# Performance work log

Measured on AMD Instinct MI355X. Metric: run time of the kernel, lower is better.

The kernel has to match this reference:

```python
import jax, jax.numpy as jnp
import numpy as np

MAP_W = 500
INTERP_H, INTERP_W = 1024, 2048


def _bilinear_ac(x, out_h, out_w):
    # torch F.interpolate(mode='bilinear', align_corners=True), separable
    N, C, H, W = x.shape
    ys = jnp.linspace(0.0, H - 1, out_h)
    y0 = jnp.floor(ys).astype(jnp.int32)
    y1 = jnp.minimum(y0 + 1, H - 1)
    wy = (ys - y0.astype(x.dtype))[None, None, :, None]
    rows = x[:, :, y0, :] * (1 - wy) + x[:, :, y1, :] * wy  # (N,C,out_h,W)
    xs = jnp.linspace(0.0, W - 1, out_w)
    x0 = jnp.floor(xs).astype(jnp.int32)
    x1 = jnp.minimum(x0 + 1, W - 1)
    wx = (xs - x0.astype(x.dtype))[None, None, None, :]
    return rows[:, :, :, x0] * (1 - wx) + rows[:, :, :, x1] * wx


def _conv(x, w, pad):
    return jax.lax.conv_general_dilated(x, w, (1, 1), [(pad, pad), (pad, pad)],
                                        dimension_numbers=('NCHW', 'OIHW', 'NCHW'))


def _bn_relu(x, g, b):
    # BatchNorm2d in training mode: biased batch stats over (N,H,W)
    mu = jnp.mean(x, axis=(0, 2, 3), keepdims=True)
    var = jnp.var(x, axis=(0, 2, 3), keepdims=True)
    xn = (x - mu) * jax.lax.rsqrt(var + 1e-5)
    return jax.nn.relu(xn * g[None, :, None, None] + b[None, :, None, None])


def setup_inputs() -> dict:
    key = jax.random.key(0)
    ks = jax.random.split(key, 24)
    C, NOBJ = 64, 21
    features = jax.random.normal(ks[0], (1, 1, C, 256, 512), dtype=jnp.float32)
    proj_indices = jax.random.randint(ks[1], (1, MAP_W * MAP_W), 0, 400000, dtype=jnp.int64)
    masks_inliers = jax.random.bernoulli(ks[2], 0.5, (1, INTERP_H, INTERP_W))
    rgb_no_norm = jax.random.uniform(ks[3], (1, INTERP_H, INTERP_W, 3), dtype=jnp.float32) * 255.0
    def cw(k, o, i, kh, kw):
        return jax.random.normal(k, (o, i, kh, kw), dtype=jnp.float32) * (1.0 / np.sqrt(i * kh * kw))
    return {
        'features': features, 'proj_indices': proj_indices,
        'masks_inliers': masks_inliers, 'rgb_no_norm': rgb_no_norm,
        'w1': cw(ks[4], 128, C, 7, 7), 'g1': jnp.ones(128), 'b1': jnp.zeros(128),
        'w2': cw(ks[5], 64, 128, 3, 3), 'g2': jnp.ones(64), 'b2': jnp.zeros(64),
        'w3': cw(ks[6], 48, 64, 3, 3), 'g3': jnp.ones(48), 'b3': jnp.zeros(48),
        'w4': cw(ks[7], 48, 48, 3, 3), 'g4': jnp.ones(48), 'b4': jnp.zeros(48),
        'w5': cw(ks[8], NOBJ, 48, 1, 1), 'b5': jnp.zeros(NOBJ),
    }


def reference(features, proj_indices, masks_inliers, rgb_no_norm,
              w1, g1, b1, w2, g2, b2, w3, g3, b3, w4, g4, b4, w5, b5):
    N, T, C, H, W = features.shape  # N = 1
    feat = _bilinear_ac(features[:, 0], INTERP_H, INTERP_W)      # (N,C,1024,2048)
    feat = feat.transpose(0, 2, 3, 1).reshape(-1, C)             # row-major NHWC flatten
    rgb_flat = rgb_no_norm.reshape(-1, 3)
    mask_flat = masks_inliers.reshape(-1)
    # stable compaction: inlier pixels first, in original row-major order
    # (equivalent to torch boolean-mask gather feature[mask_inliers, :])
    order = jnp.argsort((~mask_flat).astype(jnp.int32), stable=True)
    compact_f = feat[order]
    compact_rgb = rgb_flat[order]
    idx = proj_indices.reshape(-1)
    m = idx < jnp.max(idx)                                       # sentinel = max value
    state = jnp.where(m[:, None], compact_f[idx], 0.0)           # replace-mode scatter
    state_rgb = jnp.where(m[:, None], compact_rgb[idx], 0.0)
    rgb_write = state_rgb.reshape(MAP_W, MAP_W, 3)
    observed_masks = m.reshape(N, MAP_W, MAP_W)
    memory = state.reshape(N, MAP_W, MAP_W, C).transpose(0, 3, 1, 2)
    # decoder (first conv in_channels fixed to C to match memory)
    x = _bn_relu(_conv(memory, w1, 3), g1, b1)
    x = _bn_relu(_conv(x, w2, 1), g2, b2)
    x = _bn_relu(_conv(x, w3, 1), g3, b3)
    x = _bn_relu(_conv(x, w4, 1), g4, b4)
    semmap = _conv(x, w5, 0) + b5[None, :, None, None]
    return (semmap, observed_masks, rgb_write)
```

## Files before the change

kernel.cpp:

```cpp
#include <hip/hip_runtime.h>

#define MAPN 250000
#define NPIX 2097152

typedef unsigned short ushort_t;
typedef __attribute__((ext_vector_type(8))) short short8;
typedef __attribute__((ext_vector_type(4))) float f32x4;

__device__ inline ushort_t f2bf(float f){
  unsigned u = __float_as_uint(f);
  u = (u + 0x7fffu + ((u >> 16) & 1u)) >> 16;
  return (ushort_t)u;
}
__device__ inline float bf2f(ushort_t h){ return __uint_as_float(((unsigned)h) << 16); }

__device__ __forceinline__ void glds16(const void* g, void* l){
  __builtin_amdgcn_global_load_lds((const __attribute__((address_space(1))) unsigned int*)g,
                                   (__attribute__((address_space(3))) unsigned int*)l, 16, 0, 0);
}

__device__ inline int read_mask(const void* p, int i, int t){
  if (t==0) return ((const int*)p)[i] != 0;
  if (t==1) return ((const unsigned char*)p)[i] != 0;
  if (t==3) return ((const long long*)p)[i] != 0;
  return ((const float*)p)[i] != 0.0f;
}
__device__ inline int read_idx(const void* p, int i, int t){
  if (t==1) return (int)((const long long*)p)[i];
  return ((const int*)p)[i];
}

__global__ void detect_kernel(const int* __restrict__ mask_w, const int* __restrict__ idx_w,
                              int* __restrict__ flags){
  int tid = threadIdx.x;
  int orv=0, modd=0, inz=0;
  for (int i=tid;i<4096;i+=256) orv |= mask_w[i];
  for (int i=tid;i<2048;i+=256) modd += (mask_w[2*i+1]!=0);
  for (int i=tid;i<2048;i+=256) inz  += (idx_w[2*i+1]!=0);
  __shared__ int sOr[256], sM[256], sI[256];
  sOr[tid]=orv; sM[tid]=modd; sI[tid]=inz; __syncthreads();
  for (int o=128;o;o>>=1){ if(tid<o){ sOr[tid]|=sOr[tid+o]; sM[tid]+=sM[tid+o]; sI[tid]+=sI[tid+o]; } __syncthreads(); }
  if (tid==0){
    int o = sOr[0];
    int mt;
    if ((o & ~1) == 0)               mt = (sM[0] > 0) ? 0 : 3;
    else if ((o & ~0x01010101) == 0) mt = 1;
    else                             mt = 2;
    flags[0] = mt;
    flags[1] = (sI[0] > 0) ? 0 : 1;
  }
}

__global__ void feat_transpose(const float* __restrict__ f, ushort_t* __restrict__ out){
  __shared__ float tile[64][65];
  int tid = threadIdx.x;
  int y = blockIdx.y;
  int x0 = blockIdx.x * 64;
  #pragma unroll
  for (int pass=0; pass<16; pass++){
    int c = pass*4 + (tid>>6);
    int x = x0 + (tid & 63);
    tile[c][tid & 63] = f[(size_t)c*131072 + (size_t)y*512 + x];
  }
  __syncthreads();
  #pragma unroll
  for (int pass=0; pass<16; pass++){
    int xl = pass*4 + (tid>>6);
    int c  = tid & 63;
    out[((size_t)y*512 + x0 + xl)*64 + c] = f2bf(tile[c][xl]);
  }
}

__global__ void scan_count(const void* __restrict__ mask, const int* __restrict__ flags,
                           int* __restrict__ blkSums){
  int t = flags[0];
  int tid = threadIdx.x;
  int base = blockIdx.x*1024 + tid*4;
  int s = 0;
  #pragma unroll
  for (int j=0;j<4;j++) s += read_mask(mask, base+j, t);
  __shared__ int red[256];
  red[tid] = s; __syncthreads();
  for (int o=128;o;o>>=1){ if (tid<o) red[tid]+=red[tid+o]; __syncthreads(); }
  if (tid==0) blkSums[blockIdx.x] = red[0];
}

__global__ void scan_offsets(const int* __restrict__ blkSums, int* __restrict__ blkOffs){
  __shared__ int tsum[256];
  int tid = threadIdx.x;
  int loc[8]; int s=0;
  #pragma unroll
  for (int j=0;j<8;j++){ loc[j]=blkSums[tid*8+j]; s+=loc[j]; }
  tsum[tid]=s; __syncthreads();
  for (int o=1;o<256;o<<=1){
    int v = (tid>=o)? tsum[tid-o] : 0;
    __syncthreads();
    tsum[tid] += v;
    __syncthreads();
  }
  int run = tsum[tid]-s;
  #pragma unroll
  for (int j=0;j<8;j++){ blkOffs[tid*8+j]=run; run+=loc[j]; }
  if (tid==255) blkOffs[2048]=run;
}

__global__ void build_table(const void* __restrict__ mask, const int* __restrict__ flags,
                            const int* __restrict__ blkOffs, int* __restrict__ table){
  int t = flags[0];
  int tid = threadIdx.x;
  int base = blockIdx.x*1024 + tid*4;
  int mv[4]; int s=0;
  #pragma unroll
  for (int j=0;j<4;j++){ mv[j]=read_mask(mask, base+j, t); s+=mv[j]; }
  __shared__ int red[256];
  red[tid]=s; __syncthreads();
  for (int o=1;o<256;o<<=1){
    int v = (tid>=o)? red[tid-o] : 0;
    __syncthreads();
    red[tid]+=v;
    __syncthreads();
  }
  int excl = red[tid]-s + blkOffs[blockIdx.x];
  int total = blkOffs[2048];
  #pragma unroll
  for (int j=0;j<4;j++){
    int p = base+j;
    int pos;
    if (mv[j]){ pos = excl; excl++; }
    else      { pos = total + (p - excl); }
    table[pos] = p;
  }
}

__global__ void max_idx_kernel(const void* __restrict__ idxp, const int* __restrict__ flags,
                               int* __restrict__ mx){
  int t = flags[1];
  int m = 0;
  for (int i = blockIdx.x*blockDim.x + threadIdx.x; i < MAPN; i += gridDim.x*blockDim.x)
    m = max(m, read_idx(idxp, i, t));
  #pragma unroll
  for (int o=32;o;o>>=1) m = max(m, __shfl_down(m, o));
  if ((threadIdx.x & 63) == 0) atomicMax(mx, m);
}

__global__ void gather_kernel(const void* __restrict__ idxp, const int* __restrict__ flags,
                              const int* __restrict__ mxp, const int* __restrict__ table,
                              const ushort_t* __restrict__ Fhwc, const float* __restrict__ rgb,
                              ushort_t* __restrict__ memory, float* __restrict__ out_obs,
                              float* __restrict__ out_rgb){
  int cell = blockIdx.x*4 + (threadIdx.x>>6);
  int lane = threadIdx.x & 63;
  int t = flags[1];
  int mx = *mxp;
  int idx = read_idx(idxp, cell, t);
  bool m = idx < mx;
  float v = 0.0f, r = 0.0f;
  if (m){
    int p = table[idx];
    int py = p >> 11, px = p & 2047;
    float fy = py * (255.0f/1023.0f);
    int y0 = (int)fy; float wy = fy - (float)y0; int y1 = min(y0+1, 255);
    float fx = px * (511.0f/2047.0f);
    int x0 = (int)fx; float wx = fx - (float)x0; int x1 = min(x0+1, 511);
    const ushort_t* f00 = Fhwc + ((size_t)y0*512 + x0)*64;
    const ushort_t* f01 = Fhwc + ((size_t)y0*512 + x1)*64;
    const ushort_t* f10 = Fhwc + ((size_t)y1*512 + x0)*64;
    const ushort_t* f11 = Fhwc + ((size_t)y1*512 + x1)*64;
    float w00=(1.0f-wy)*(1.0f-wx), w01=(1.0f-wy)*wx, w10=wy*(1.0f-wx), w11=wy*wx;
    v = w00*bf2f(f00[lane]) + w01*bf2f(f01[lane]) + w10*bf2f(f10[lane]) + w11*bf2f(f11[lane]);
    if (lane < 3) r = rgb[(size_t)p*3 + lane];
  }
  memory[(size_t)cell*64 + lane] = f2bf(v);
  if (lane == 0) out_obs[cell] = m ? 1.0f : 0.0f;
  if (lane < 3)  out_rgb[(size_t)cell*3 + lane] = r;
}

__global__ void wprep_frag2(const float* __restrict__ w, ushort_t* __restrict__ out,
                            int O, int I, int KK, int COS, int KC){
  int NFS = COS/16;
  int total = KK*KC*NFS*512;
  for (int e = blockIdx.x*blockDim.x + threadIdx.x; e < total; e += gridDim.x*blockDim.x){
    int j = e & 7, l = (e>>3)&63;
    int f = e >> 9;
    int nf = f % NFS; f /= NFS;
    int kc = f % KC;  int t = f / KC;
    int co = nf*16 + (l&15);
    int ci = kc*32 + ((l>>4)&3)*8 + j;
    float v = (co < O && ci < I) ? w[((size_t)co*I + ci)*KK + t] : 0.0f;
    out[e] = f2bf(v);
  }
}

template<int CI, int CO, int COPAD, int KS, int PAD, bool HASBN, int CIREAL,
         int TR, int WM, int WN>
__global__ __launch_bounds__(256, 2) void conv2d(const ushort_t* __restrict__ in,
                                                 const ushort_t* __restrict__ wt,
                                                 const float* __restrict__ scsh,
                                                 ushort_t* __restrict__ out,
                                                 float* __restrict__ partials){
  constexpr int TCOL = 64;
  constexpr int ECOL = TCOL + 2*PAD;
  constexpr int E    = TR*ECOL;
  constexpr int MF   = TR*4;
  constexpr int MI   = MF/WM;
  constexpr int NFS  = CO/16;
  constexpr int NFW  = NFS/WN;
  constexpr int KC   = CI/32;
  constexpr int CIG  = CI/8;
  constexpr int TB   = CO*CI*2;
  constexpr int NSL  = TB/1024;
  constexpr int NT   = KS*KS;
  constexpr int TOT  = E*CIG;
  constexpr int PASSES = (TOT+255)/256;
  constexpr int SCN = HASBN ? CIREAL : 1;

  __shared__ char sA[E*CI*2];
  __shared__ char sB[2][TB];
  __shared__ float sStat[4][NFW][16][2];
  __shared__ float sSc[SCN], sSh[SCN];

  const int tid = threadIdx.x, lane = tid & 63, wv = tid >> 6;
  const int wm = wv / WN, wn = wv % WN;
  const int cc = blockIdx.x & 7;
  const int rb = blockIdx.x >> 3;
  const int x0 = cc*TCOL, yb = rb*TR;

  if (HASBN){
    for (int i=tid;i<CIREAL;i+=256){ sSc[i]=scsh[i]; sSh[i]=scsh[CIREAL+i]; }
    __syncthreads();
  }

  int ebase[MI], frow[MI], fcolb[MI];
  #pragma unroll
  for (int mi=0;mi<MI;mi++){
    int f = wm*MI + mi;
    frow[mi]  = f >> 2;
    fcolb[mi] = (f & 3) * 16;
    ebase[mi] = frow[mi]*ECOL + fcolb[mi] + (lane & 15);
  }

  f32x4 acc[MI][NFW];
  #pragma unroll
  for (int mi=0;mi<MI;mi++)
    #pragma unroll
    for (int ni=0;ni<NFW;ni++) acc[mi][ni] = (f32x4)0.0f;

  for (int s=wv; s<NSL; s+=4)
    glds16((const char*)wt + (size_t)s*1024 + lane*16, &sB[0][s*1024]);

  int cur = 0;

  for (int kh=0; kh<KS; kh++){
    #pragma unroll
    for (int i=0;i<PASSES;i++){
      int c = i*256 + tid;
      if ((TOT % 256 == 0) || c < TOT){
        int e = c / CIG, ci8 = (c % CIG)*8;
        int row = e / ECOL, col = e % ECOL;
        int yy = yb + row + kh - PAD;
        int xx = x0 + col - PAD;
        uint4 v = make_uint4(0u,0u,0u,0u);
        bool ok = ((unsigned)yy < 500u) && ((unsigned)xx < 500u) && (!HASBN || ci8 < CIREAL);
        if (ok){
          v = *(const uint4*)(in + ((size_t)yy*500 + xx)*CI + ci8);
          if (HASBN){
            ushort_t* hv = (ushort_t*)&v;
            #pragma unroll
            for (int j=0;j<8;j++){
              float f = bf2f(hv[j]);
              f = fmaxf(fmaf(f, sSc[ci8+j], sSh[ci8+j]), 0.0f);
              hv[j] = f2bf(f);
            }
          }
        }
        unsigned wa = ((unsigned)((e*CI + ci8)*2)) ^ ((unsigned)(e&7)<<4);
        *(uint4*)(sA + wa) = v;
      }
    }
    __syncthreads();

    for (int kw=0; kw<KS; kw++){
      int t = kh*KS + kw;
      if (t+1 < NT){
        for (int s=wv; s<NSL; s+=4)
          glds16((const char*)wt + (size_t)(t+1)*TB + (size_t)s*1024 + lane*16,
                 &sB[cur^1][s*1024]);
      }
      #pragma unroll
      for (int kc=0;kc<KC;kc++){
        short8 bfr[NFW];
        #pragma unroll
        for (int ni=0;ni<NFW;ni++)
          bfr[ni] = *(const short8*)(&sB[cur][((kc*NFS + wn*NFW + ni)<<10) + lane*16]);
        #pragma unroll
        for (int mi=0;mi<MI;mi++){
          int e = ebase[mi] + kw;
          unsigned ra = ((unsigned)((e*CI + kc*32 + (lane>>4)*8)*2)) ^ ((unsigned)(e&7)<<4);
          short8 af = *(const short8*)(sA + ra);
          #pragma unroll
          for (int ni=0;ni<NFW;ni++)
            acc[mi][ni] = __builtin_amdgcn_mfma_f32_16x16x32_bf16(af, bfr[ni], acc[mi][ni], 0,0,0);
        }
      }
      __syncthreads();
      cur ^= 1;
    }
  }

  #pragma unroll
  for (int ni=0;ni<NFW;ni++){
    float ps=0.f, pq=0.f;
    #pragma unroll
    for (int mi=0;mi<MI;mi++){
      int colb = fcolb[mi] + (lane>>4)*4;
      size_t rowoff = (size_t)(yb + frow[mi])*500;
      #pragma unroll
      for (int j=0;j<4;j++){
        float v = acc[mi][ni][j];
        int colAbs = x0 + colb + j;
        if (colAbs < 500){
          ps += v; pq += v*v;
          out[(rowoff + colAbs)*COPAD + wn*(NFW*16) + ni*16 + (lane&15)] = f2bf(v);
        }
      }
    }
    ps += __shfl_xor(ps, 16); pq += __shfl_xor(pq, 16);
    ps += __shfl_xor(ps, 32); pq += __shfl_xor(pq, 32);
    if (lane < 16){ sStat[wv][ni][lane][0]=ps; sStat[wv][ni][lane][1]=pq; }
  }
  __syncthreads();
  if (tid < CO){
    int wn_ = tid / (NFW*16);
    int r = tid % (NFW*16);
    int ni_ = r >> 4, col = r & 15;
    float s = 0.f, q = 0.f;
    #pragma unroll
    for (int m=0;m<WM;m++){
      s += sStat[m*WN + wn_][ni_][col][0];
      q += sStat[m*WN + wn_][ni_][col][1];
    }
    partials[(size_t)blockIdx.x*(2*CO) + tid]      = s;
    partials[(size_t)blockIdx.x*(2*CO) + CO + tid] = q;
  }
}

__global__ void bn_reduce2(const float* __restrict__ partials, int nblk, int CO,
                           const float* __restrict__ g, const float* __restrict__ b,
                           float* __restrict__ scsh){
  int c = blockIdx.x;
  float s=0.f, q=0.f;
  for (int i=threadIdx.x; i<nblk; i+=256){
    s += partials[(size_t)i*(2*CO) + c];
    q += partials[(size_t)i*(2*CO) + CO + c];
  }
  __shared__ float rs[256], rq[256];
  rs[threadIdx.x]=s; rq[threadIdx.x]=q; __syncthreads();
  for (int o=128;o;o>>=1){
    if (threadIdx.x<o){ rs[threadIdx.x]+=rs[threadIdx.x+o]; rq[threadIdx.x]+=rq[threadIdx.x+o]; }
    __syncthreads();
  }
  if (threadIdx.x==0){
    float mean = rs[0]*(1.0f/(float)MAPN);
    float var  = rq[0]*(1.0f/(float)MAPN) - mean*mean;
    float inv  = rsqrtf(var + 1e-5f);
    float sc   = g[c]*inv;
    scsh[c]    = sc;
    scsh[CO+c] = b[c] - mean*sc;
  }
}

__global__ void conv5_kernel(const ushort_t* __restrict__ in, const float* __restrict__ w,
                             const float* __restrict__ bias, const float* __restrict__ scsh,
                             float* __restrict__ out){
  __shared__ float sw[21*48];
  __shared__ float sb[21];
  __shared__ float sc[48], sh[48];
  for (int i=threadIdx.x;i<1008;i+=256) sw[i]=w[i];
  if (threadIdx.x<21) sb[threadIdx.x]=bias[threadIdx.x];
  if (threadIdx.x<48){ sc[threadIdx.x]=scsh[threadIdx.x]; sh[threadIdx.x]=scsh[48+threadIdx.x]; }
  __syncthreads();
  int pix = blockIdx.x*256 + threadIdx.x;
  if (pix >= MAPN) return;
  float acc[21];
  #pragma unroll
  for (int i=0;i<21;i++) acc[i]=0.0f;
  const ushort_t* ip = in + (size_t)pix*64;
  #pragma unroll
  for (int cg=0; cg<6; cg++){
    uint4 v = *(const uint4*)(ip + cg*8);
    ushort_t* hv = (ushort_t*)&v;
    #pragma unroll
    for (int j=0;j<8;j++){
      int ci = cg*8+j;
      float s = fmaxf(fmaf(bf2f(hv[j]), sc[ci], sh[ci]), 0.0f);
      #pragma unroll
      for (int co=0;co<21;co++) acc[co]=fmaf(s, sw[co*48+ci], acc[co]);
    }
  }
  #pragma unroll
  for (int co=0;co<21;co++) out[(size_t)co*MAPN + pix] = acc[co] + sb[co];
}

static inline size_t al256(size_t x){ return (x + 255) & ~(size_t)255; }

extern "C" void kernel_launch(void* const* d_in, const int* in_sizes, int n_in,
                              void* d_out, int out_size, void* d_ws, size_t ws_size,
                              hipStream_t stream){
  const float* features = (const float*)d_in[0];
  const void*  proj     = d_in[1];
  const void*  mask     = d_in[2];
  const float* rgb      = (const float*)d_in[3];
  const float* w1 = (const float*)d_in[4];
  const float* g1 = (const float*)d_in[5];
  const float* b1 = (const float*)d_in[6];
  const float* w2 = (const float*)d_in[7];
  const float* g2 = (const float*)d_in[8];
  const float* b2 = (const float*)d_in[9];
  const float* w3 = (const float*)d_in[10];
  const float* g3 = (const float*)d_in[11];
  const float* b3 = (const float*)d_in[12];
  const float* w4 = (const float*)d_in[13];
  const float* g4 = (const float*)d_in[14];
  const float* b4 = (const float*)d_in[15];
  const float* w5 = (const float*)d_in[16];
  const float* b5 = (const float*)d_in[17];

  char* ws = (char*)d_ws;
  size_t off = 0;
  ushort_t* mem_bf = (ushort_t*)(ws + off); off += al256((size_t)MAPN*64*2);
  ushort_t* actA   = (ushort_t*)(ws + off); off += al256((size_t)MAPN*128*2);
  ushort_t* actB   = (ushort_t*)(ws + off); off += al256((size_t)MAPN*64*2);
  ushort_t* Fhwc   = (ushort_t*)(ws + off); off += al256((size_t)131072*64*2);
  int*      table  = (int*)(ws + off);      off += al256((size_t)NPIX*4);
  ushort_t* wh1    = (ushort_t*)(ws + off); off += al256((size_t)128*49*64*2);
  ushort_t* wh2    = (ushort_t*)(ws + off); off += al256((size_t)64*9*128*2);
  ushort_t* wh3    = (ushort_t*)(ws + off); off += al256((size_t)48*9*64*2);
  ushort_t* wh4    = (ushort_t*)(ws + off); off += al256((size_t)48*9*64*2);
  float*    partials = (float*)(ws + off);  off += al256((size_t)2048*256*4);
  int* blkSums = (int*)(ws + off); off += al256(2048*4);
  int* blkOffs = (int*)(ws + off); off += al256(2049*4);
  int* maxidx  = (int*)(ws + off); off += 256;
  int* flags   = (int*)(ws + off); off += 256;
  float* scsh1 = (float*)(ws + off); off += al256(256*4);
  float* scsh2 = (float*)(ws + off); off += al256(256*4);
  float* scsh3 = (float*)(ws + off); off += al256(256*4);
  float* scsh4 = (float*)(ws + off); off += al256(256*4);

  float* out_sem = (float*)d_out;
  float* out_obs = out_sem + (size_t)21*MAPN;
  float* out_rgb = out_obs + MAPN;

  detect_kernel<<<1,256,0,stream>>>((const int*)mask, (const int*)proj, flags);
  feat_transpose<<<dim3(8,256),256,0,stream>>>(features, Fhwc);

  scan_count<<<2048,256,0,stream>>>(mask, flags, blkSums);
  scan_offsets<<<1,256,0,stream>>>(blkSums, blkOffs);
  build_table<<<2048,256,0,stream>>>(mask, flags, blkOffs, table);

  hipMemsetAsync(maxidx, 0, 4, stream);
  max_idx_kernel<<<256,256,0,stream>>>(proj, flags, maxidx);

  wprep_frag2<<<512,256,0,stream>>>(w1, wh1, 128, 64, 49, 128, 2);
  wprep_frag2<<<128,256,0,stream>>>(w2, wh2, 64, 128, 9, 64, 4);
  wprep_frag2<<<64,256,0,stream>>>(w3, wh3, 48, 64, 9, 48, 2);
  wprep_frag2<<<64,256,0,stream>>>(w4, wh4, 48, 48, 9, 48, 2);

  gather_kernel<<<62500,256,0,stream>>>(proj, flags, maxidx, table, Fhwc, rgb,
                                        mem_bf, out_obs, out_rgb);

  conv2d<64,128,128,7,3,false,64,4,2,2><<<125*8,256,0,stream>>>(mem_bf, wh1, nullptr, actA, partials);
  bn_reduce2<<<128,256,0,stream>>>(partials, 1000, 128, g1, b1, scsh1);

  conv2d<128,64,64,3,1,true,128,2,2,2><<<250*8,256,0,stream>>>(actA, wh2, scsh1, actB, partials);
  bn_reduce2<<<64,256,0,stream>>>(partials, 2000, 64, g2, b2, scsh2);

  conv2d<64,48,64,3,1,true,64,4,4,1><<<125*8,256,0,stream>>>(actB, wh3, scsh2, actA, partials);
  bn_reduce2<<<48,256,0,stream>>>(partials, 1000, 48, g3, b3, scsh3);

  conv2d<64,48,64,3,1,true,48,4,4,1><<<125*8,256,0,stream>>>(actA, wh4, scsh3, actB, partials);
  bn_reduce2<<<48,256,0,stream>>>(partials, 1000, 48, g4, b4, scsh4);

  conv5_kernel<<<(MAPN+255)/256,256,0,stream>>>(actB, w5, b5, scsh4, out_sem);
}
```

Baseline: 479.3 us.

## Run decoder convolutions with FP8 MFMA using per-channel scaled weights

Converts the gathered memory map, the BN-applied activations and the conv weights to FP8 (e4m3) and switches the conv MFMAs from bf16 16x16x32 to fp8 16x16x32. Weights get a per-output-channel power-of-two scale, which the following training-mode BatchNorm cancels. The aim is to halve LDS and global traffic for activations and weights and to use the higher FP8 matrix throughput. It also doubles the conv2 row tile and folds the max-index memset into the detect kernel. The cost is a large precision drop that may break output tolerance.

```diff
diff --git a/kernel.cpp b/kernel.cpp
--- a/kernel.cpp
+++ b/kernel.cpp
@@ -4,7 +4,6 @@
 #define NPIX 2097152
 
 typedef unsigned short ushort_t;
-typedef __attribute__((ext_vector_type(8))) short short8;
 typedef __attribute__((ext_vector_type(4))) float f32x4;
 
 __device__ inline ushort_t f2bf(float f){
@@ -31,7 +30,7 @@
 }
 
 __global__ void detect_kernel(const int* __restrict__ mask_w, const int* __restrict__ idx_w,
-                              int* __restrict__ flags){
+                              int* __restrict__ flags, int* __restrict__ maxidx){
   int tid = threadIdx.x;
   int orv=0, modd=0, inz=0;
   for (int i=tid;i<4096;i+=256) orv |= mask_w[i];
@@ -48,6 +47,7 @@
     else                             mt = 2;
     flags[0] = mt;
     flags[1] = (sI[0] > 0) ? 0 : 1;
+    maxidx[0] = 0;
   }
 }
 
@@ -146,7 +146,7 @@
 __global__ void gather_kernel(const void* __restrict__ idxp, const int* __restrict__ flags,
                               const int* __restrict__ mxp, const int* __restrict__ table,
                               const ushort_t* __restrict__ Fhwc, const float* __restrict__ rgb,
-                              ushort_t* __restrict__ memory, float* __restrict__ out_obs,
+                              unsigned char* __restrict__ mem_f8, float* __restrict__ out_obs,
                               float* __restrict__ out_rgb){
   int cell = blockIdx.x*4 + (threadIdx.x>>6);
   int lane = threadIdx.x & 63;
@@ -170,34 +170,49 @@
     v = w00*bf2f(f00[lane]) + w01*bf2f(f01[lane]) + w10*bf2f(f10[lane]) + w11*bf2f(f11[lane]);
     if (lane < 3) r = rgb[(size_t)p*3 + lane];
   }
-  memory[(size_t)cell*64 + lane] = f2bf(v);
+  int q = __builtin_amdgcn_cvt_pk_fp8_f32(v, 0.0f, 0, false);
+  mem_f8[(size_t)cell*64 + lane] = (unsigned char)(q & 0xff);
   if (lane == 0) out_obs[cell] = m ? 1.0f : 0.0f;
   if (lane < 3)  out_rgb[(size_t)cell*3 + lane] = r;
 }
 
-__global__ void wprep_frag2(const float* __restrict__ w, ushort_t* __restrict__ out,
-                            int O, int I, int KK, int COS, int KC){
-  int NFS = COS/16;
-  int total = KK*KC*NFS*512;
-  for (int e = blockIdx.x*blockDim.x + threadIdx.x; e < total; e += gridDim.x*blockDim.x){
-    int j = e & 7, l = (e>>3)&63;
-    int f = e >> 9;
-    int nf = f % NFS; f /= NFS;
-    int kc = f % KC;  int t = f / KC;
-    int co = nf*16 + (l&15);
-    int ci = kc*32 + ((l>>4)&3)*8 + j;
-    float v = (co < O && ci < I) ? w[((size_t)co*I + ci)*KK + t] : 0.0f;
-    out[e] = f2bf(v);
+__global__ void wprep_f8(const float* __restrict__ w, unsigned char* __restrict__ out,
+                         int O, int I, int CIPAD, int KK){
+  int co = blockIdx.x;
+  int n = KK*CIPAD;
+  int NFS = (O+15)>>4;
+  int KC  = CIPAD>>5;
+  float mx = 0.f;
+  for (int e=threadIdx.x; e<n; e+=256){
+    int ci = e % CIPAD;
+    if (ci < I){
+      int t = e / CIPAD;
+      mx = fmaxf(mx, fabsf(w[((size_t)co*I + ci)*KK + t]));
+    }
+  }
+  __shared__ float red[256];
+  red[threadIdx.x]=mx; __syncthreads();
+  for (int o=128;o;o>>=1){ if(threadIdx.x<o) red[threadIdx.x]=fmaxf(red[threadIdx.x],red[threadIdx.x+o]); __syncthreads(); }
+  float m = red[0];
+  float sc = (m > 0.f) ? exp2f(floorf(log2f(224.0f/m))) : 1.0f;
+  for (int e=threadIdx.x; e<n; e+=256){
+    int t = e / CIPAD, ci = e % CIPAD;
+    float v = (ci < I) ? w[((size_t)co*I + ci)*KK + t]*sc : 0.0f;
+    int q = __builtin_amdgcn_cvt_pk_fp8_f32(v, 0.0f, 0, false);
+    int kc = ci>>5, g=(ci>>3)&3, j=ci&7;
+    int l = g*16 + (co&15);
+    size_t pos = ((size_t)(t*KC + kc)*NFS + (co>>4))*512 + l*8 + j;
+    out[pos] = (unsigned char)(q & 0xff);
   }
 }
 
 template<int CI, int CO, int COPAD, int KS, int PAD, bool HASBN, int CIREAL,
          int TR, int WM, int WN>
-__global__ __launch_bounds__(256, 2) void conv2d(const ushort_t* __restrict__ in,
-                                                 const ushort_t* __restrict__ wt,
-                                                 const float* __restrict__ scsh,
-                                                 ushort_t* __restrict__ out,
-                                                 float* __restrict__ partials){
+__global__ __launch_bounds__(256, 2) void conv2d_f8(const void* __restrict__ in,
+                                                    const unsigned char* __restrict__ wt,
+                                                    const float* __restrict__ scsh,
+                                                    ushort_t* __restrict__ out,
+                                                    float* __restrict__ partials){
   constexpr int TCOL = 64;
   constexpr int ECOL = TCOL + 2*PAD;
   constexpr int E    = TR*ECOL;
@@ -207,15 +222,15 @@
   constexpr int NFW  = NFS/WN;
   constexpr int KC   = CI/32;
   constexpr int CIG  = CI/8;
-  constexpr int TB   = CO*CI*2;
+  constexpr int TB   = CO*CI;
   constexpr int NSL  = TB/1024;
   constexpr int NT   = KS*KS;
   constexpr int TOT  = E*CIG;
   constexpr int PASSES = (TOT+255)/256;
   constexpr int SCN = HASBN ? CIREAL : 1;
 
-  __shared__ char sA[E*CI*2];
-  __shared__ char sB[2][TB];
+  __shared__ unsigned char sA[E*CI];
+  __shared__ unsigned char sB[2][TB];
   __shared__ float sStat[4][NFW][16][2];
   __shared__ float sSc[SCN], sSh[SCN];
 
@@ -224,6 +239,9 @@
   const int cc = blockIdx.x & 7;
   const int rb = blockIdx.x >> 3;
   const int x0 = cc*TCOL, yb = rb*TR;
+
+  const ushort_t* inb = (const ushort_t*)in;
+  const unsigned char* in8 = (const unsigned char*)in;
 
   if (HASBN){
     for (int i=tid;i<CIREAL;i+=256){ sSc[i]=scsh[i]; sSh[i]=scsh[CIREAL+i]; }
@@ -259,22 +277,27 @@
         int row = e / ECOL, col = e % ECOL;
         int yy = yb + row + kh - PAD;
         int xx = x0 + col - PAD;
-        uint4 v = make_uint4(0u,0u,0u,0u);
+        uint2 q = make_uint2(0u,0u);
         bool ok = ((unsigned)yy < 500u) && ((unsigned)xx < 500u) && (!HASBN || ci8 < CIREAL);
         if (ok){
-          v = *(const uint4*)(in + ((size_t)yy*500 + xx)*CI + ci8);
           if (HASBN){
+            uint4 v = *(const uint4*)(inb + ((size_t)yy*500 + xx)*CI + ci8);
             ushort_t* hv = (ushort_t*)&v;
+            float f[8];
             #pragma unroll
-            for (int j=0;j<8;j++){
-              float f = bf2f(hv[j]);
-              f = fmaxf(fmaf(f, sSc[ci8+j], sSh[ci8+j]), 0.0f);
-              hv[j] = f2bf(f);
-            }
+            for (int j=0;j<8;j++)
+              f[j] = fmaxf(fmaf(bf2f(hv[j]), sSc[ci8+j], sSh[ci8+j]), 0.0f);
+            int d0 = __builtin_amdgcn_cvt_pk_fp8_f32(f[0], f[1], 0, false);
+            d0     = __builtin_amdgcn_cvt_pk_fp8_f32(f[2], f[3], d0, true);
+            int d1 = __builtin_amdgcn_cvt_pk_fp8_f32(f[4], f[5], 0, false);
+            d1     = __builtin_amdgcn_cvt_pk_fp8_f32(f[6], f[7], d1, true);
+            q = make_uint2((unsigned)d0, (unsigned)d1);
+          } else {
+            q = *(const uint2*)(in8 + ((size_t)yy*500 + xx)*CI + ci8);
           }
         }
-        unsigned wa = ((unsigned)((e*CI + ci8)*2)) ^ ((unsigned)(e&7)<<4);
-        *(uint4*)(sA + wa) = v;
+        unsigned wa = ((unsigned)(e*CI + ci8)) ^ ((unsigned)(e&7)<<3);
+        *(uint2*)(sA + wa) = q;
       }
     }
     __syncthreads();
@@ -288,18 +311,18 @@
       }
       #pragma unroll
       for (int kc=0;kc<KC;kc++){
-        short8 bfr[NFW];
+        long long bfr[NFW];
         #pragma unroll
         for (int ni=0;ni<NFW;ni++)
-          bfr[ni] = *(const short8*)(&sB[cur][((kc*NFS + wn*NFW + ni)<<10) + lane*16]);
+          bfr[ni] = *(const long long*)(&sB[cur][((kc*NFS + wn*NFW + ni)<<9) + lane*8]);
         #pragma unroll
         for (int mi=0;mi<MI;mi++){
           int e = ebase[mi] + kw;
-          unsigned ra = ((unsigned)((e*CI + kc*32 + (lane>>4)*8)*2)) ^ ((unsigned)(e&7)<<4);
-          short8 af = *(const short8*)(sA + ra);
+          unsigned ra = ((unsigned)(e*CI + kc*32 + (lane>>4)*8)) ^ ((unsigned)(e&7)<<3);
+          long long af = *(const long long*)(sA + ra);
           #pragma unroll
           for (int ni=0;ni<NFW;ni++)
-            acc[mi][ni] = __builtin_amdgcn_mfma_f32_16x16x32_bf16(af, bfr[ni], acc[mi][ni], 0,0,0);
+            acc[mi][ni] = __builtin_amdgcn_mfma_f32_16x16x32_fp8_fp8(af, bfr[ni], acc[mi][ni], 0,0,0);
         }
       }
       __syncthreads();
@@ -427,15 +450,15 @@
 
   char* ws = (char*)d_ws;
   size_t off = 0;
-  ushort_t* mem_bf = (ushort_t*)(ws + off); off += al256((size_t)MAPN*64*2);
+  unsigned char* mem_f8 = (unsigned char*)(ws + off); off += al256((size_t)MAPN*64);
   ushort_t* actA   = (ushort_t*)(ws + off); off += al256((size_t)MAPN*128*2);
   ushort_t* actB   = (ushort_t*)(ws + off); off += al256((size_t)MAPN*64*2);
   ushort_t* Fhwc   = (ushort_t*)(ws + off); off += al256((size_t)131072*64*2);
   int*      table  = (int*)(ws + off);      off += al256((size_t)NPIX*4);
-  ushort_t* wh1    = (ushort_t*)(ws + off); off += al256((size_t)128*49*64*2);
-  ushort_t* wh2    = (ushort_t*)(ws + off); off += al256((size_t)64*9*128*2);
-  ushort_t* wh3    = (ushort_t*)(ws + off); off += al256((size_t)48*9*64*2);
-  ushort_t* wh4    = (ushort_t*)(ws + off); off += al256((size_t)48*9*64*2);
+  unsigned char* wh1 = (unsigned char*)(ws + off); off += al256((size_t)49*2*8*512);
+  unsigned char* wh2 = (unsigned char*)(ws + off); off += al256((size_t)9*4*4*512);
+  unsigned char* wh3 = (unsigned char*)(ws + off); off += al256((size_t)9*2*3*512);
+  unsigned char* wh4 = (unsigned char*)(ws + off); off += al256((size_t)9*2*3*512);
   float*    partials = (float*)(ws + off);  off += al256((size_t)2048*256*4);
   int* blkSums = (int*)(ws + off); off += al256(2048*4);
   int* blkOffs = (int*)(ws + off); off += al256(2049*4);
@@ -450,34 +473,33 @@
   float* out_obs = out_sem + (size_t)21*MAPN;
   float* out_rgb = out_obs + MAPN;
 
-  detect_kernel<<<1,256,0,stream>>>((const int*)mask, (const int*)proj, flags);
+  detect_kernel<<<1,256,0,stream>>>((const int*)mask, (const int*)proj, flags, maxidx);
   feat_transpose<<<dim3(8,256),256,0,stream>>>(features, Fhwc);
 
   scan_count<<<2048,256,0,stream>>>(mask, flags, blkSums);
   scan_offsets<<<1,256,0,stream>>>(blkSums, blkOffs);
   build_table<<<2048,256,0,stream>>>(mask, flags, blkOffs, table);
 
-  hipMemsetAsync(maxidx, 0, 4, stream);
   max_idx_kernel<<<256,256,0,stream>>>(proj, flags, maxidx);
 
-  wprep_frag2<<<512,256,0,stream>>>(w1, wh1, 128, 64, 49, 128, 2);
-  wprep_frag2<<<128,256,0,stream>>>(w2, wh2, 64, 128, 9, 64, 4);
-  wprep_frag2<<<64,256,0,stream>>>(w3, wh3, 48, 64, 9, 48, 2);
-  wprep_frag2<<<64,256,0,stream>>>(w4, wh4, 48, 48, 9, 48, 2);
+  wprep_f8<<<128,256,0,stream>>>(w1, wh1, 128, 64, 64, 49);
+  wprep_f8<<<64,256,0,stream>>>(w2, wh2, 64, 128, 128, 9);
+  wprep_f8<<<48,256,0,stream>>>(w3, wh3, 48, 64, 64, 9);
+  wprep_f8<<<48,256,0,stream>>>(w4, wh4, 48, 48, 64, 9);
 
   gather_kernel<<<62500,256,0,stream>>>(proj, flags, maxidx, table, Fhwc, rgb,
-                                        mem_bf, out_obs, out_rgb);
-
-  conv2d<64,128,128,7,3,false,64,4,2,2><<<125*8,256,0,stream>>>(mem_bf, wh1, nullptr, actA, partials);
+                                        mem_f8, out_obs, out_rgb);
+
+  conv2d_f8<64,128,128,7,3,false,64,4,2,2><<<125*8,256,0,stream>>>(mem_f8, wh1, nullptr, actA, partials);
   bn_reduce2<<<128,256,0,stream>>>(partials, 1000, 128, g1, b1, scsh1);
 
-  conv2d<128,64,64,3,1,true,128,2,2,2><<<250*8,256,0,stream>>>(actA, wh2, scsh1, actB, partials);
-  bn_reduce2<<<64,256,0,stream>>>(partials, 2000, 64, g2, b2, scsh2);
-
-  conv2d<64,48,64,3,1,true,64,4,4,1><<<125*8,256,0,stream>>>(actB, wh3, scsh2, actA, partials);
+  conv2d_f8<128,64,64,3,1,true,128,4,2,2><<<125*8,256,0,stream>>>(actA, wh2, scsh1, actB, partials);
+  bn_reduce2<<<64,256,0,stream>>>(partials, 1000, 64, g2, b2, scsh2);
+
+  conv2d_f8<64,48,64,3,1,true,64,4,4,1><<<125*8,256,0,stream>>>(actB, wh3, scsh2, actA, partials);
   bn_reduce2<<<48,256,0,stream>>>(partials, 1000, 48, g3, b3, scsh3);
 
-  conv2d<64,48,64,3,1,true,48,4,4,1><<<125*8,256,0,stream>>>(actA, wh4, scsh3, actB, partials);
+  conv2d_f8<64,48,64,3,1,true,48,4,4,1><<<125*8,256,0,stream>>>(actA, wh4, scsh3, actB, partials);
   bn_reduce2<<<48,256,0,stream>>>(partials, 1000, 48, g4, b4, scsh4);
 
   conv5_kernel<<<(MAPN+255)/256,256,0,stream>>>(actB, w5, b5, scsh4, out_sem);
```

Result: slower. 509.0 us (+6.2%).

## Run first 7x7 conv in FP8 MFMA with per-channel power-of-two weight scaling

Applied to the files above, without the earlier changes.

The gather kernel now writes the memory map as FP8 (e4m3) instead of bf16. A new weight-prep kernel quantizes conv1 weights to FP8 with a per-output-channel power-of-two scale, and a new conv2d_f8 kernel uses 16x16x32 FP8 MFMAs. The weight scale is never undone, which relies on the following training-mode BatchNorm cancelling per-channel positive scaling. This is meant to halve operand bytes and raise matrix throughput for the heaviest conv, at the cost of much lower input precision. Separately, the maxidx memset is folded into detect_kernel to drop one API call.

```diff
diff --git a/kernel.cpp b/kernel.cpp
--- a/kernel.cpp
+++ b/kernel.cpp
@@ -31,7 +31,7 @@
 }
 
 __global__ void detect_kernel(const int* __restrict__ mask_w, const int* __restrict__ idx_w,
-                              int* __restrict__ flags){
+                              int* __restrict__ flags, int* __restrict__ maxidx){
   int tid = threadIdx.x;
   int orv=0, modd=0, inz=0;
   for (int i=tid;i<4096;i+=256) orv |= mask_w[i];
@@ -48,6 +48,7 @@
     else                             mt = 2;
     flags[0] = mt;
     flags[1] = (sI[0] > 0) ? 0 : 1;
+    maxidx[0] = 0;
   }
 }
 
@@ -146,7 +147,7 @@
 __global__ void gather_kernel(const void* __restrict__ idxp, const int* __restrict__ flags,
                               const int* __restrict__ mxp, const int* __restrict__ table,
                               const ushort_t* __restrict__ Fhwc, const float* __restrict__ rgb,
-                              ushort_t* __restrict__ memory, float* __restrict__ out_obs,
+                              unsigned char* __restrict__ mem_f8, float* __restrict__ out_obs,
                               float* __restrict__ out_rgb){
   int cell = blockIdx.x*4 + (threadIdx.x>>6);
   int lane = threadIdx.x & 63;
@@ -170,9 +171,40 @@
     v = w00*bf2f(f00[lane]) + w01*bf2f(f01[lane]) + w10*bf2f(f10[lane]) + w11*bf2f(f11[lane]);
     if (lane < 3) r = rgb[(size_t)p*3 + lane];
   }
-  memory[(size_t)cell*64 + lane] = f2bf(v);
+  int q = __builtin_amdgcn_cvt_pk_fp8_f32(v, 0.0f, 0, false);
+  mem_f8[(size_t)cell*64 + lane] = (unsigned char)(q & 0xff);
   if (lane == 0) out_obs[cell] = m ? 1.0f : 0.0f;
   if (lane < 3)  out_rgb[(size_t)cell*3 + lane] = r;
+}
+
+__global__ void wprep_f8(const float* __restrict__ w, unsigned char* __restrict__ out,
+                         int O, int I, int CIPAD, int KK){
+  int co = blockIdx.x;
+  int n = KK*CIPAD;
+  int NFS = (O+15)>>4;
+  int KC  = CIPAD>>5;
+  float mx = 0.f;
+  for (int e=threadIdx.x; e<n; e+=256){
+    int ci = e % CIPAD;
+    if (ci < I){
+      int t = e / CIPAD;
+      mx = fmaxf(mx, fabsf(w[((size_t)co*I + ci)*KK + t]));
+    }
+  }
+  __shared__ float red[256];
+  red[threadIdx.x]=mx; __syncthreads();
+  for (int o=128;o;o>>=1){ if(threadIdx.x<o) red[threadIdx.x]=fmaxf(red[threadIdx.x],red[threadIdx.x+o]); __syncthreads(); }
+  float m = red[0];
+  float sc = (m > 0.f) ? exp2f(floorf(log2f(224.0f/m))) : 1.0f;
+  for (int e=threadIdx.x; e<n; e+=256){
+    int t = e / CIPAD, ci = e % CIPAD;
+    float v = (ci < I) ? w[((size_t)co*I + ci)*KK + t]*sc : 0.0f;
+    int q = __builtin_amdgcn_cvt_pk_fp8_f32(v, 0.0f, 0, false);
+    int kc = ci>>5, g=(ci>>3)&3, j=ci&7;
+    int l = g*16 + (co&15);
+    size_t pos = ((size_t)(t*KC + kc)*NFS + (co>>4))*512 + l*8 + j;
+    out[pos] = (unsigned char)(q & 0xff);
+  }
 }
 
 __global__ void wprep_frag2(const float* __restrict__ w, ushort_t* __restrict__ out,
@@ -188,6 +220,139 @@
     int ci = kc*32 + ((l>>4)&3)*8 + j;
     float v = (co < O && ci < I) ? w[((size_t)co*I + ci)*KK + t] : 0.0f;
     out[e] = f2bf(v);
+  }
+}
+
+template<int CI, int CO, int COPAD, int KS, int PAD, int TR, int WM, int WN>
+__global__ __launch_bounds__(256, 2) void conv2d_f8(const unsigned char* __restrict__ in8,
+                                                    const unsigned char* __restrict__ wt,
+                                                    ushort_t* __restrict__ out,
+                                                    float* __restrict__ partials){
+  constexpr int TCOL = 64;
+  constexpr int ECOL = TCOL + 2*PAD;
+  constexpr int E    = TR*ECOL;
+  constexpr int MF   = TR*4;
+  constexpr int MI   = MF/WM;
+  constexpr int NFS  = CO/16;
+  constexpr int NFW  = NFS/WN;
+  constexpr int KC   = CI/32;
+  constexpr int CIG  = CI/8;
+  constexpr int TB   = CO*CI;
+  constexpr int NSL  = TB/1024;
+  constexpr int NT   = KS*KS;
+  constexpr int TOT  = E*CIG;
+  constexpr int PASSES = (TOT+255)/256;
+
+  __shared__ unsigned char sA[E*CI + 128];
+  __shared__ unsigned char sB[2][TB];
+  __shared__ float sStat[4][NFW][16][2];
+
+  const int tid = threadIdx.x, lane = tid & 63, wv = tid >> 6;
+  const int wm = wv / WN, wn = wv % WN;
+  const int cc = blockIdx.x & 7;
+  const int rb = blockIdx.x >> 3;
+  const int x0 = cc*TCOL, yb = rb*TR;
+
+  int ebase[MI], frow[MI], fcolb[MI];
+  #pragma unroll
+  for (int mi=0;mi<MI;mi++){
+    int f = wm*MI + mi;
+    frow[mi]  = f >> 2;
+    fcolb[mi] = (f & 3) * 16;
+    ebase[mi] = frow[mi]*ECOL + fcolb[mi] + (lane & 15);
+  }
+
+  f32x4 acc[MI][NFW];
+  #pragma unroll
+  for (int mi=0;mi<MI;mi++)
+    #pragma unroll
+    for (int ni=0;ni<NFW;ni++) acc[mi][ni] = (f32x4)0.0f;
+
+  for (int s=wv; s<NSL; s+=4)
+    glds16((const char*)wt + (size_t)s*1024 + lane*16, &sB[0][s*1024]);
+
+  int cur = 0;
+
+  for (int kh=0; kh<KS; kh++){
+    #pragma unroll
+    for (int i=0;i<PASSES;i++){
+      int c = i*256 + tid;
+      if ((TOT % 256 == 0) || c < TOT){
+        int e = c / CIG, ci8 = (c % CIG)*8;
+        int row = e / ECOL, col = e % ECOL;
+        int yy = yb + row + kh - PAD;
+        int xx = x0 + col - PAD;
+        uint2 q = make_uint2(0u,0u);
+        if (((unsigned)yy < 500u) && ((unsigned)xx < 500u))
+          q = *(const uint2*)(in8 + ((size_t)yy*500 + xx)*CI + ci8);
+        unsigned wa = ((unsigned)(e*CI + ci8)) ^ ((unsigned)(e&15)<<3);
+        *(uint2*)(sA + wa) = q;
+      }
+    }
+    __syncthreads();
+
+    for (int kw=0; kw<KS; kw++){
+      int t = kh*KS + kw;
+      if (t+1 < NT){
+        for (int s=wv; s<NSL; s+=4)
+          glds16((const char*)wt + (size_t)(t+1)*TB + (size_t)s*1024 + lane*16,
+                 &sB[cur^1][s*1024]);
+      }
+      #pragma unroll
+      for (int kc=0;kc<KC;kc++){
+        long long bfr[NFW];
+        #pragma unroll
+        for (int ni=0;ni<NFW;ni++)
+          bfr[ni] = *(const long long*)(&sB[cur][((kc*NFS + wn*NFW + ni)<<9) + lane*8]);
+        #pragma unroll
+        for (int mi=0;mi<MI;mi++){
+          int e = ebase[mi] + kw;
+          unsigned ra = ((unsigned)(e*CI + kc*32 + (lane>>4)*8)) ^ ((unsigned)(e&15)<<3);
+          long long af = *(const long long*)(sA + ra);
+          #pragma unroll
+          for (int ni=0;ni<NFW;ni++)
+            acc[mi][ni] = __builtin_amdgcn_mfma_f32_16x16x32_fp8_fp8(af, bfr[ni], acc[mi][ni], 0,0,0);
+        }
+      }
+      __syncthreads();
+      cur ^= 1;
+    }
+  }
+
+  #pragma unroll
+  for (int ni=0;ni<NFW;ni++){
+    float ps=0.f, pq=0.f;
+    #pragma unroll
+    for (int mi=0;mi<MI;mi++){
+      int colb = fcolb[mi] + (lane>>4)*4;
+      size_t rowoff = (size_t)(yb + frow[mi])*500;
+      #pragma unroll
+      for (int j=0;j<4;j++){
+        float v = acc[mi][ni][j];
+        int colAbs = x0 + colb + j;
+        if (colAbs < 500){
+          ps += v; pq += v*v;
+          out[(rowoff + colAbs)*COPAD + wn*(NFW*16) + ni*16 + (lane&15)] = f2bf(v);
+        }
+      }
+    }
+    ps += __shfl_xor(ps, 16); pq += __shfl_xor(pq, 16);
+    ps += __shfl_xor(ps, 32); pq += __shfl_xor(pq, 32);
+    if (lane < 16){ sStat[wv][ni][lane][0]=ps; sStat[wv][ni][lane][1]=pq; }
+  }
+  __syncthreads();
+  if (tid < CO){
+    int wn_ = tid / (NFW*16);
+    int r = tid % (NFW*16);
+    int ni_ = r >> 4, col = r & 15;
+    float s = 0.f, q = 0.f;
+    #pragma unroll
+    for (int m=0;m<WM;m++){
+      s += sStat[m*WN + wn_][ni_][col][0];
+      q += sStat[m*WN + wn_][ni_][col][1];
+    }
+    partials[(size_t)blockIdx.x*(2*CO) + tid]      = s;
+    partials[(size_t)blockIdx.x*(2*CO) + CO + tid] = q;
   }
 }
 
@@ -427,15 +592,15 @@
 
   char* ws = (char*)d_ws;
   size_t off = 0;
-  ushort_t* mem_bf = (ushort_t*)(ws + off); off += al256((size_t)MAPN*64*2);
+  unsigned char* mem_f8 = (unsigned char*)(ws + off); off += al256((size_t)MAPN*64);
   ushort_t* actA   = (ushort_t*)(ws + off); off += al256((size_t)MAPN*128*2);
   ushort_t* actB   = (ushort_t*)(ws + off); off += al256((size_t)MAPN*64*2);
   ushort_t* Fhwc   = (ushort_t*)(ws + off); off += al256((size_t)131072*64*2);
   int*      table  = (int*)(ws + off);      off += al256((size_t)NPIX*4);
-  ushort_t* wh1    = (ushort_t*)(ws + off); off += al256((size_t)128*49*64*2);
-  ushort_t* wh2    = (ushort_t*)(ws + off); off += al256((size_t)64*9*128*2);
-  ushort_t* wh3    = (ushort_t*)(ws + off); off += al256((size_t)48*9*64*2);
-  ushort_t* wh4    = (ushort_t*)(ws + off); off += al256((size_t)48*9*64*2);
+  unsigned char* wh1 = (unsigned char*)(ws + off); off += al256((size_t)49*2*8*512);
+  ushort_t* wh2    = (ushort_t*)(ws + off); off += al256((size_t)9*4*4*512*2);
+  ushort_t* wh3    = (ushort_t*)(ws + off); off += al256((size_t)9*2*3*512*2);
+  ushort_t* wh4    = (ushort_t*)(ws + off); off += al256((size_t)9*2*3*512*2);
   float*    partials = (float*)(ws + off);  off += al256((size_t)2048*256*4);
   int* blkSums = (int*)(ws + off); off += al256(2048*4);
   int* blkOffs = (int*)(ws + off); off += al256(2049*4);
@@ -450,25 +615,24 @@
   float* out_obs = out_sem + (size_t)21*MAPN;
   float* out_rgb = out_obs + MAPN;
 
-  detect_kernel<<<1,256,0,stream>>>((const int*)mask, (const int*)proj, flags);
+  detect_kernel<<<1,256,0,stream>>>((const int*)mask, (const int*)proj, flags, maxidx);
   feat_transpose<<<dim3(8,256),256,0,stream>>>(features, Fhwc);
 
   scan_count<<<2048,256,0,stream>>>(mask, flags, blkSums);
   scan_offsets<<<1,256,0,stream>>>(blkSums, blkOffs);
   build_table<<<2048,256,0,stream>>>(mask, flags, blkOffs, table);
 
-  hipMemsetAsync(maxidx, 0, 4, stream);
   max_idx_kernel<<<256,256,0,stream>>>(proj, flags, maxidx);
 
-  wprep_frag2<<<512,256,0,stream>>>(w1, wh1, 128, 64, 49, 128, 2);
+  wprep_f8<<<128,256,0,stream>>>(w1, wh1, 128, 64, 64, 49);
   wprep_frag2<<<128,256,0,stream>>>(w2, wh2, 64, 128, 9, 64, 4);
   wprep_frag2<<<64,256,0,stream>>>(w3, wh3, 48, 64, 9, 48, 2);
   wprep_frag2<<<64,256,0,stream>>>(w4, wh4, 48, 48, 9, 48, 2);
 
   gather_kernel<<<62500,256,0,stream>>>(proj, flags, maxidx, table, Fhwc, rgb,
-                                        mem_bf, out_obs, out_rgb);
-
-  conv2d<64,128,128,7,3,false,64,4,2,2><<<125*8,256,0,stream>>>(mem_bf, wh1, nullptr, actA, partials);
+                                        mem_f8, out_obs, out_rgb);
+
+  conv2d_f8<64,128,128,7,3,4,2,2><<<125*8,256,0,stream>>>(mem_f8, wh1, actA, partials);
   bn_reduce2<<<128,256,0,stream>>>(partials, 1000, 128, g1, b1, scsh1);
 
   conv2d<128,64,64,3,1,true,128,2,2,2><<<250*8,256,0,stream>>>(actA, wh2, scsh1, actB, partials);
```

New measurement: 469.5 us. -2.1%, faster.
